# Kernel optimization log

Hardware: AMD Instinct MI355X
Metric: run time of the kernel (lower is better)

## Reference

```python
import jax, jax.numpy as jnp
import numpy as np

B, H, W, C = 8, 224, 224, 96
WS, SHIFT, HEADS = 7, 3, 3
N = WS * WS
HEAD_DIM = C // HEADS
SCALE = HEAD_DIM ** -0.5
EPS = 1e-5


def _build_shift_mask():
    # standard Swin shifted-window attention mask, values in {0, -100}
    img = np.zeros((H, W), np.float32)
    cnt = 0
    for hs in (slice(0, -WS), slice(-WS, -SHIFT), slice(-SHIFT, None)):
        for ws_ in (slice(0, -WS), slice(-WS, -SHIFT), slice(-SHIFT, None)):
            img[hs, ws_] = cnt
            cnt += 1
    mw = img.reshape(H // WS, WS, W // WS, WS).transpose(0, 2, 1, 3).reshape(-1, N)  # (nW, N)
    am = mw[:, None, :] - mw[:, :, None]
    am = np.where(am != 0, -100.0, 0.0).astype(np.float32)  # (nW, N, N)
    return np.tile(am, (B, 1, 1))  # (B*nW, N, N)


def setup_inputs() -> dict:
    key = jax.random.key(0)
    ks = jax.random.split(key, 6)
    s = 0.02
    return {
        "x": jax.random.normal(ks[0], (B, H, W, C), jnp.float32),
        "mask": jnp.asarray(_build_shift_mask()),
        "norm1_g": jnp.ones((C,), jnp.float32),
        "norm1_b": jnp.zeros((C,), jnp.float32),
        "qkv_w": jax.random.normal(ks[1], (3 * C, C), jnp.float32) * s,
        "qkv_b": jnp.zeros((3 * C,), jnp.float32),
        "proj_w": jax.random.normal(ks[2], (C, C), jnp.float32) * s,
        "proj_b": jnp.zeros((C,), jnp.float32),
        "norm2_g": jnp.ones((C,), jnp.float32),
        "norm2_b": jnp.zeros((C,), jnp.float32),
        "fc1_w": jax.random.normal(ks[3], (4 * C, C), jnp.float32) * s,
        "fc1_b": jnp.zeros((4 * C,), jnp.float32),
        "fc2_w": jax.random.normal(ks[4], (C, 4 * C), jnp.float32) * s,
        "fc2_b": jnp.zeros((C,), jnp.float32),
    }


def _ln(x, g, b):
    mu = jnp.mean(x, axis=-1, keepdims=True)
    var = jnp.mean(jnp.square(x - mu), axis=-1, keepdims=True)
    return (x - mu) * jax.lax.rsqrt(var + EPS) * g + b


def reference(x, mask, norm1_g, norm1_b, qkv_w, qkv_b, proj_w, proj_b,
              norm2_g, norm2_b, fc1_w, fc1_b, fc2_w, fc2_b):
    b, h, w, c = x.shape
    shortcut = x.reshape(b, h * w, c)
    xn = _ln(x, norm1_g, norm1_b)
    # cyclic shift
    xs = jnp.roll(xn, (-SHIFT, -SHIFT), axis=(1, 2))
    # window partition -> (B*nW, N, C)
    xw = xs.reshape(b, h // WS, WS, w // WS, WS, c).transpose(0, 1, 3, 2, 4, 5).reshape(-1, N, c)
    # window attention
    qkv = xw @ qkv_w.T + qkv_b                                  # (B_, N, 3C)
    qkv = qkv.reshape(-1, N, 3, HEADS, HEAD_DIM).transpose(2, 0, 3, 1, 4)
    q, k, v = qkv[0] * SCALE, qkv[1], qkv[2]                    # (B_, h, N, d)
    attn = jnp.einsum('bhnd,bhmd->bhnm', q, k) + mask[:, None]  # (B_, h, N, N)
    attn = jax.nn.softmax(attn, axis=-1)
    o = jnp.einsum('bhnm,bhmd->bhnd', attn, v).transpose(0, 2, 1, 3).reshape(-1, N, c)
    o = o @ proj_w.T + proj_b
    # window reverse
    o = o.reshape(b, h // WS, w // WS, WS, WS, c).transpose(0, 1, 3, 2, 4, 5).reshape(b, h, w, c)
    o = jnp.roll(o, (SHIFT, SHIFT), axis=(1, 2)).reshape(b, h * w, c)
    x = shortcut + o
    # MLP with exact (erf) GELU, as torch nn.GELU default
    y = _ln(x, norm2_g, norm2_b)
    y = jax.nn.gelu(y @ fc1_w.T + fc1_b, approximate=False)
    return x + (y @ fc2_w.T + fc2_b)
```

## Files before the change

kernel.cpp:

```cpp
#include <hip/hip_runtime.h>

typedef __attribute__((ext_vector_type(8))) short short8;
typedef __attribute__((ext_vector_type(4))) float floatx4;

#define MFMA(a,b,c) __builtin_amdgcn_mfma_f32_16x16x32_bf16(a,b,c,0,0,0)

__device__ __forceinline__ ushort f2bf(float f){ union{float f;uint i;}x; x.f=f; return (ushort)((x.i + 0x7fffu + ((x.i>>16)&1u))>>16); }
__device__ __forceinline__ short8 lds8(const ushort* p){ return *(const short8*)p; }

__global__ void convw_kernel(const float* __restrict__ qkvw,
                             const float* __restrict__ projw,
                             const float* __restrict__ f1w,
                             const float* __restrict__ f2w,
                             ushort* __restrict__ wb)
{
  int i = blockIdx.x*256 + threadIdx.x;
  float v;
  if      (i < 27648)  v = qkvw[i];
  else if (i < 36864)  v = projw[i-27648];
  else if (i < 73728)  v = f1w[i-36864];
  else if (i < 110592) v = f2w[i-73728];
  else return;
  wb[i] = f2bf(v);
}

__global__ __launch_bounds__(256,4) void swin_block_kernel(
    const float* __restrict__ x,
    const float* __restrict__ g1, const float* __restrict__ b1v,
    const ushort* __restrict__ qkv_wb, const float* __restrict__ qkv_b,
    const ushort* __restrict__ proj_wb, const float* __restrict__ proj_b,
    const float* __restrict__ g2, const float* __restrict__ b2v,
    const ushort* __restrict__ fc1_wb, const float* __restrict__ fc1_b,
    const ushort* __restrict__ fc2_wb, const float* __restrict__ fc2_b,
    float* __restrict__ out)
{
  __shared__ __align__(16) ushort sm[19200];
  __shared__ int sid[64];
  ushort* xn  = sm;
  ushort* Qh  = sm + 6656;
  ushort* Kh  = sm + 8704;
  ushort* Vh  = sm + 11264;
  ushort* Pb  = sm + 13568;
  float*  xrb = (float*)(sm + 6656);
  ushort* hb  = sm + 6656;

  const int tid  = threadIdx.x;
  const int w    = blockIdx.x;
  const int b    = w >> 10;
  const int wh   = (w >> 5) & 31;
  const int wwn  = w & 31;
  const int lane = tid & 63;
  const int wv   = tid >> 6;
  const int quad = lane >> 4;
  const int ln   = lane & 15;

  {
    const int n = tid >> 2, q = tid & 3;
    if (n < 49) {
      const int i = n / 7, j = n - 7*i;
      int hh = wh*7 + i + 3; if (hh >= 224) hh -= 224;
      int w2 = wwn*7 + j + 3; if (w2 >= 224) w2 -= 224;
      if (q == 0) {
        const int rr = (wh < 31) ? 0 : ((i < 4) ? 1 : 2);
        const int cr = (wwn < 31) ? 0 : ((j < 4) ? 1 : 2);
        sid[n] = rr*3 + cr;
      }
      const float* px = x + (((size_t)b*224 + hh)*224 + w2)*96 + q*24;
      float v[24]; float s = 0.f, s2 = 0.f;
      const float4* p4 = (const float4*)px;
      #pragma unroll
      for (int t = 0; t < 6; ++t) { float4 u = p4[t];
        v[t*4+0]=u.x; v[t*4+1]=u.y; v[t*4+2]=u.z; v[t*4+3]=u.w; }
      #pragma unroll
      for (int c = 0; c < 24; ++c) { s += v[c]; s2 += v[c]*v[c]; }
      s  += __shfl_xor(s, 1);  s  += __shfl_xor(s, 2);
      s2 += __shfl_xor(s2, 1); s2 += __shfl_xor(s2, 2);
      const float mu = s * (1.f/96.f);
      const float rs = rsqrtf(s2*(1.f/96.f) - mu*mu + 1e-5f);
      ushort* row = xn + n*104 + q*24;
      #pragma unroll
      for (int c = 0; c < 24; ++c)
        row[c] = f2bf((v[c]-mu)*rs*g1[q*24+c] + b1v[q*24+c]);
    }
    for (int idx = tid; idx < 15*104; idx += 256) xn[49*104 + idx] = 0;
  }
  __syncthreads();

  short8 a0, a1, a2;
  {
    const ushort* arow = xn + (wv*16 + ln)*104 + quad*8;
    a0 = lds8(arow); a1 = lds8(arow+32); a2 = lds8(arow+64);
  }
  int idrv[4], idcv[4];
  #pragma unroll
  for (int reg = 0; reg < 4; ++reg) {
    const int r = wv*16 + quad*4 + reg;
    idrv[reg] = (r < 49) ? sid[r] : -1;
  }
  #pragma unroll
  for (int nt = 0; nt < 4; ++nt) {
    const int c = nt*16 + ln;
    idcv[nt] = (c < 49) ? sid[c] : -2;
  }

  ushort* ob = xn;
  for (int h = 0; h < 3; ++h) {
    #pragma unroll
    for (int nt = 0; nt < 6; ++nt) {
      const int sec = nt >> 1, sub = nt & 1;
      const int colw = sec*96 + h*32 + sub*16 + ln;
      const ushort* wrow = qkv_wb + colw*96 + quad*8;
      floatx4 acc = {0.f,0.f,0.f,0.f};
      acc = MFMA(a0, lds8(wrow),    acc);
      acc = MFMA(a1, lds8(wrow+32), acc);
      acc = MFMA(a2, lds8(wrow+64), acc);
      const float bias = qkv_b[colw];
      const int d = sub*16 + ln;
      #pragma unroll
      for (int reg = 0; reg < 4; ++reg) {
        const int r = wv*16 + quad*4 + reg;
        float val = acc[reg] + bias;
        if (sec == 0)      Qh[r*32 + d] = f2bf(val * 0.17677669529663689f);
        else if (sec == 1) Kh[r*40 + d] = f2bf(val);
        else               Vh[d*72 + r] = f2bf(val);
      }
    }
    __syncthreads();

    {
      short8 aq = lds8(Qh + (wv*16 + ln)*32 + quad*8);
      floatx4 sc[4];
      #pragma unroll
      for (int nt = 0; nt < 4; ++nt) {
        short8 kb = lds8(Kh + (nt*16 + ln)*40 + quad*8);
        floatx4 z = {0.f,0.f,0.f,0.f};
        sc[nt] = MFMA(aq, kb, z);
      }
      #pragma unroll
      for (int reg = 0; reg < 4; ++reg) {
        float t[4]; float mx = -1e30f;
        #pragma unroll
        for (int nt = 0; nt < 4; ++nt) {
          float tv = -1e30f;
          if (idrv[reg] >= 0 && idcv[nt] >= 0)
            tv = sc[nt][reg] + ((idrv[reg] == idcv[nt]) ? 0.f : -100.f);
          t[nt] = tv; mx = fmaxf(mx, tv);
        }
        mx = fmaxf(mx, __shfl_xor(mx, 1));
        mx = fmaxf(mx, __shfl_xor(mx, 2));
        mx = fmaxf(mx, __shfl_xor(mx, 4));
        mx = fmaxf(mx, __shfl_xor(mx, 8));
        float e[4], sum = 0.f;
        #pragma unroll
        for (int nt = 0; nt < 4; ++nt) {
          e[nt] = (t[nt] > -1e29f) ? __expf(t[nt] - mx) : 0.f;
          sum += e[nt];
        }
        sum += __shfl_xor(sum, 1);
        sum += __shfl_xor(sum, 2);
        sum += __shfl_xor(sum, 4);
        sum += __shfl_xor(sum, 8);
        const float inv = (sum > 0.f) ? 1.f/sum : 0.f;
        #pragma unroll
        for (int nt = 0; nt < 4; ++nt)
          Pb[(wv*16 + quad*4 + reg)*72 + nt*16 + ln] = f2bf(e[nt]*inv);
      }
    }
    __syncthreads();

    {
      short8 p0 = lds8(Pb + (wv*16 + ln)*72 + quad*8);
      short8 p1 = lds8(Pb + (wv*16 + ln)*72 + 32 + quad*8);
      #pragma unroll
      for (int ntd = 0; ntd < 2; ++ntd) {
        floatx4 accO = {0.f,0.f,0.f,0.f};
        accO = MFMA(p0, lds8(Vh + (ntd*16+ln)*72 + quad*8),      accO);
        accO = MFMA(p1, lds8(Vh + (ntd*16+ln)*72 + 32 + quad*8), accO);
        #pragma unroll
        for (int reg = 0; reg < 4; ++reg)
          ob[(wv*16 + quad*4 + reg)*104 + h*32 + ntd*16 + ln] = f2bf(accO[reg]);
      }
    }
    __syncthreads();
  }

  {
    const ushort* arow = ob + (wv*16 + ln)*104 + quad*8;
    short8 o0 = lds8(arow), o1 = lds8(arow+32), o2 = lds8(arow+64);
    for (int nt = 0; nt < 6; ++nt) {
      const ushort* wrow = proj_wb + (nt*16 + ln)*96 + quad*8;
      floatx4 acc = {0.f,0.f,0.f,0.f};
      acc = MFMA(o0, lds8(wrow),    acc);
      acc = MFMA(o1, lds8(wrow+32), acc);
      acc = MFMA(o2, lds8(wrow+64), acc);
      const int col = nt*16 + ln;
      const float bias = proj_b[col];
      #pragma unroll
      for (int reg = 0; reg < 4; ++reg) {
        const int r = wv*16 + quad*4 + reg;
        if (r < 49) {
          const int i = r / 7, j = r - 7*i;
          int hh = wh*7 + i + 3; if (hh >= 224) hh -= 224;
          int w2 = wwn*7 + j + 3; if (w2 >= 224) w2 -= 224;
          const size_t pos = (((size_t)b*224 + hh)*224 + w2)*96 + col;
          const float val = x[pos] + acc[reg] + bias;
          xrb[r*96 + col] = val;
          out[pos] = val;
        }
      }
    }
    for (int idx = tid; idx < 15*96; idx += 256) xrb[49*96 + idx] = 0.f;
  }
  __syncthreads();

  {
    const int n = tid >> 2, q = tid & 3;
    const float4* p4 = (const float4*)(xrb + n*96 + q*24);
    float v[24]; float s = 0.f, s2 = 0.f;
    #pragma unroll
    for (int t = 0; t < 6; ++t) { float4 u = p4[t];
      v[t*4+0]=u.x; v[t*4+1]=u.y; v[t*4+2]=u.z; v[t*4+3]=u.w; }
    #pragma unroll
    for (int c = 0; c < 24; ++c) { s += v[c]; s2 += v[c]*v[c]; }
    s  += __shfl_xor(s, 1);  s  += __shfl_xor(s, 2);
    s2 += __shfl_xor(s2, 1); s2 += __shfl_xor(s2, 2);
    const float mu = s * (1.f/96.f);
    const float rs = rsqrtf(s2*(1.f/96.f) - mu*mu + 1e-5f);
    ushort* row = xn + n*104 + q*24;
    #pragma unroll
    for (int c = 0; c < 24; ++c)
      row[c] = f2bf((v[c]-mu)*rs*g2[q*24+c] + b2v[q*24+c]);
  }
  __syncthreads();

  const int rloc = (wv & 1) * 16;
  const int p    = wv >> 1;
  for (int half = 0; half < 2; ++half) {
    {
      const ushort* arow = xn + (half*32 + rloc + ln)*104 + quad*8;
      short8 m0 = lds8(arow), m1 = lds8(arow+32), m2 = lds8(arow+64);
      for (int t = 0; t < 12; ++t) {
        const int nt = p*12 + t;
        const ushort* wrow = fc1_wb + (nt*16 + ln)*96 + quad*8;
        floatx4 acc = {0.f,0.f,0.f,0.f};
        acc = MFMA(m0, lds8(wrow),    acc);
        acc = MFMA(m1, lds8(wrow+32), acc);
        acc = MFMA(m2, lds8(wrow+64), acc);
        const int col = nt*16 + ln;
        const float bias = fc1_b[col];
        #pragma unroll
        for (int reg = 0; reg < 4; ++reg) {
          const float vv = acc[reg] + bias;
          hb[(rloc + quad*4 + reg)*392 + col] =
              f2bf(0.5f*vv*(1.f + erff(vv*0.70710678118654752f)));
        }
      }
    }
    __syncthreads();
    {
      short8 ap[12];
      const ushort* prow = hb + (rloc + ln)*392 + quad*8;
      #pragma unroll
      for (int kt = 0; kt < 12; ++kt) ap[kt] = lds8(prow + kt*32);
      for (int t = 0; t < 3; ++t) {
        const int nt = p*3 + t;
        const ushort* wrow = fc2_wb + (nt*16 + ln)*384 + quad*8;
        floatx4 acc = {0.f,0.f,0.f,0.f};
        #pragma unroll
        for (int kt = 0; kt < 12; ++kt) acc = MFMA(ap[kt], lds8(wrow + kt*32), acc);
        const int col = nt*16 + ln;
        const float bias = fc2_b[col];
        #pragma unroll
        for (int reg = 0; reg < 4; ++reg) {
          const int r = half*32 + rloc + quad*4 + reg;
          if (r < 49) {
            const int i = r / 7, j = r - 7*i;
            int hh = wh*7 + i + 3; if (hh >= 224) hh -= 224;
            int w2 = wwn*7 + j + 3; if (w2 >= 224) w2 -= 224;
            const size_t pos = (((size_t)b*224 + hh)*224 + w2)*96 + col;
            out[pos] += acc[reg] + bias;
          }
        }
      }
    }
    __syncthreads();
  }
}

extern "C" void kernel_launch(void* const* d_in, const int* in_sizes, int n_in,
                              void* d_out, int out_size, void* d_ws, size_t ws_size,
                              hipStream_t stream) {
  int ix=-1, iq=-1, ip=-1, if1=-1, if2=-1, largest=0;
  for (int i = 0; i < n_in; ++i) {
    const int s = in_sizes[i];
    if (s == 38535168 && ix < 0) ix = i;
    else if (s == 27648 && iq < 0) iq = i;
    else if (s == 9216 && ip < 0) ip = i;
    else if (s == 36864) { if (if1 < 0) if1 = i; else if (if2 < 0) if2 = i; }
    if (in_sizes[i] >= in_sizes[largest]) largest = i;
  }
  if (ix < 0) ix = largest;
  if (iq < 0) iq = 4;
  if (ip < 0) ip = 6;
  if (if1 < 0) if1 = 10;
  if (if2 < 0) if2 = 12;

  const float* x    = (const float*)d_in[ix];
  const float* n1g  = (const float*)d_in[2];
  const float* n1b  = (const float*)d_in[3];
  const float* qkvw = (const float*)d_in[iq];
  const float* qkvb = (const float*)d_in[5];
  const float* pw   = (const float*)d_in[ip];
  const float* pb   = (const float*)d_in[7];
  const float* n2g  = (const float*)d_in[8];
  const float* n2b  = (const float*)d_in[9];
  const float* f1w  = (const float*)d_in[if1];
  const float* f1b  = (const float*)d_in[11];
  const float* f2w  = (const float*)d_in[if2];
  const float* f2b  = (const float*)d_in[13];
  float* outp = (float*)d_out;
  ushort* wb = (ushort*)d_ws;

  convw_kernel<<<432, 256, 0, stream>>>(qkvw, pw, f1w, f2w, wb);
  swin_block_kernel<<<8192, 256, 0, stream>>>(
      x, n1g, n1b, wb, qkvb, wb + 27648, pb,
      n2g, n2b, wb + 36864, f1b, wb + 73728, f2b, outp);
}
```

Baseline: 927.3 us.

## Re-tile GEMMs so each wave owns weight columns and reuses B fragments across row tiles

The QKV, proj, fc1 and fc2 GEMMs are restructured. Each wave now keeps all activation row-tiles in registers and loads each weight fragment once, reusing it across four row tiles, instead of reloading weights for every row tile. The MLP is split into two hidden chunks that accumulate fc2 results in registers, so out is read-modify-written only once and hb shrinks. Global output offsets are precomputed into shared memory. The cost is higher register pressure from 12-fragment arrays and accumulators, which may reduce occupancy under launch_bounds(256,4), plus some uneven work across waves for the V and proj tail tiles.

Measured after the change: 961.1 us. 1.04x slower.

```diff
diff --git a/kernel.cpp b/kernel.cpp
--- a/kernel.cpp
+++ b/kernel.cpp
@@ -34,13 +34,14 @@
     const ushort* __restrict__ fc2_wb, const float* __restrict__ fc2_b,
     float* __restrict__ out)
 {
-  __shared__ __align__(16) ushort sm[19200];
+  __shared__ __align__(16) ushort sm[19456];
   __shared__ int sid[64];
+  __shared__ int spos[64];
   ushort* xn  = sm;
   ushort* Qh  = sm + 6656;
-  ushort* Kh  = sm + 8704;
-  ushort* Vh  = sm + 11264;
-  ushort* Pb  = sm + 13568;
+  ushort* Kh  = sm + 9216;
+  ushort* Vh  = sm + 11776;
+  ushort* Pb  = sm + 14080;
   float*  xrb = (float*)(sm + 6656);
   ushort* hb  = sm + 6656;
 
@@ -63,9 +64,10 @@
       if (q == 0) {
         const int rr = (wh < 31) ? 0 : ((i < 4) ? 1 : 2);
         const int cr = (wwn < 31) ? 0 : ((j < 4) ? 1 : 2);
-        sid[n] = rr*3 + cr;
-      }
-      const float* px = x + (((size_t)b*224 + hh)*224 + w2)*96 + q*24;
+        sid[n]  = rr*3 + cr;
+        spos[n] = ((b*224 + hh)*224 + w2)*96;
+      }
+      const float* px = x + (size_t)(((b*224 + hh)*224 + w2)*96) + q*24;
       float v[24]; float s = 0.f, s2 = 0.f;
       const float4* p4 = (const float4*)px;
       #pragma unroll
@@ -86,11 +88,13 @@
   }
   __syncthreads();
 
-  short8 a0, a1, a2;
-  {
-    const ushort* arow = xn + (wv*16 + ln)*104 + quad*8;
-    a0 = lds8(arow); a1 = lds8(arow+32); a2 = lds8(arow+64);
-  }
+  short8 a_[12];
+  #pragma unroll
+  for (int rt = 0; rt < 4; ++rt)
+    #pragma unroll
+    for (int k = 0; k < 3; ++k)
+      a_[rt*3+k] = lds8(xn + (rt*16 + ln)*104 + k*32 + quad*8);
+
   int idrv[4], idcv[4];
   #pragma unroll
   for (int reg = 0; reg < 4; ++reg) {
@@ -105,30 +109,51 @@
 
   ushort* ob = xn;
   for (int h = 0; h < 3; ++h) {
-    #pragma unroll
-    for (int nt = 0; nt < 6; ++nt) {
-      const int sec = nt >> 1, sub = nt & 1;
+    {
+      const int sec  = wv >> 1;
+      const int sub  = wv & 1;
       const int colw = sec*96 + h*32 + sub*16 + ln;
-      const ushort* wrow = qkv_wb + colw*96 + quad*8;
-      floatx4 acc = {0.f,0.f,0.f,0.f};
-      acc = MFMA(a0, lds8(wrow),    acc);
-      acc = MFMA(a1, lds8(wrow+32), acc);
-      acc = MFMA(a2, lds8(wrow+64), acc);
-      const float bias = qkv_b[colw];
-      const int d = sub*16 + ln;
-      #pragma unroll
-      for (int reg = 0; reg < 4; ++reg) {
-        const int r = wv*16 + quad*4 + reg;
-        float val = acc[reg] + bias;
-        if (sec == 0)      Qh[r*32 + d] = f2bf(val * 0.17677669529663689f);
-        else if (sec == 1) Kh[r*40 + d] = f2bf(val);
-        else               Vh[d*72 + r] = f2bf(val);
+      const ushort* wr = qkv_wb + colw*96 + quad*8;
+      short8 b0 = lds8(wr), b1 = lds8(wr+32), b2 = lds8(wr+64);
+      const int colv = 192 + h*32 + (wv>>1)*16 + ln;
+      const ushort* wr2 = qkv_wb + colv*96 + quad*8;
+      short8 c0 = lds8(wr2), c1 = lds8(wr2+32), c2 = lds8(wr2+64);
+      const float biasA = qkv_b[colw];
+      const float biasV = qkv_b[colv];
+      const int d  = sub*16 + ln;
+      const int dv = (wv>>1)*16 + ln;
+      #pragma unroll
+      for (int rt = 0; rt < 4; ++rt) {
+        floatx4 acc = {0.f,0.f,0.f,0.f};
+        acc = MFMA(a_[rt*3+0], b0, acc);
+        acc = MFMA(a_[rt*3+1], b1, acc);
+        acc = MFMA(a_[rt*3+2], b2, acc);
+        #pragma unroll
+        for (int reg = 0; reg < 4; ++reg) {
+          const int r = rt*16 + quad*4 + reg;
+          const float val = acc[reg] + biasA;
+          if (sec == 0) Qh[r*40 + d] = f2bf(val * 0.17677669529663689f);
+          else          Kh[r*40 + d] = f2bf(val);
+        }
+      }
+      const int rt0 = (wv & 1)*2;
+      #pragma unroll
+      for (int j = 0; j < 2; ++j) {
+        floatx4 acc = {0.f,0.f,0.f,0.f};
+        acc = MFMA(a_[(rt0+j)*3+0], c0, acc);
+        acc = MFMA(a_[(rt0+j)*3+1], c1, acc);
+        acc = MFMA(a_[(rt0+j)*3+2], c2, acc);
+        #pragma unroll
+        for (int reg = 0; reg < 4; ++reg) {
+          const int r = (rt0+j)*16 + quad*4 + reg;
+          Vh[dv*72 + r] = f2bf(acc[reg] + biasV);
+        }
       }
     }
     __syncthreads();
 
     {
-      short8 aq = lds8(Qh + (wv*16 + ln)*32 + quad*8);
+      short8 aq = lds8(Qh + (wv*16 + ln)*40 + quad*8);
       floatx4 sc[4];
       #pragma unroll
       for (int nt = 0; nt < 4; ++nt) {
@@ -185,26 +210,52 @@
   }
 
   {
-    const ushort* arow = ob + (wv*16 + ln)*104 + quad*8;
-    short8 o0 = lds8(arow), o1 = lds8(arow+32), o2 = lds8(arow+64);
-    for (int nt = 0; nt < 6; ++nt) {
-      const ushort* wrow = proj_wb + (nt*16 + ln)*96 + quad*8;
+    short8 o_[12];
+    #pragma unroll
+    for (int rt = 0; rt < 4; ++rt)
+      #pragma unroll
+      for (int k = 0; k < 3; ++k)
+        o_[rt*3+k] = lds8(ob + (rt*16 + ln)*104 + k*32 + quad*8);
+
+    const int colA = wv*16 + ln;
+    const ushort* wr = proj_wb + colA*96 + quad*8;
+    short8 b0 = lds8(wr), b1 = lds8(wr+32), b2 = lds8(wr+64);
+    const int colB = (4 + (wv>>1))*16 + ln;
+    const ushort* wr2 = proj_wb + colB*96 + quad*8;
+    short8 c0 = lds8(wr2), c1 = lds8(wr2+32), c2 = lds8(wr2+64);
+    const float biasA = proj_b[colA], biasB = proj_b[colB];
+
+    #pragma unroll
+    for (int rt = 0; rt < 4; ++rt) {
       floatx4 acc = {0.f,0.f,0.f,0.f};
-      acc = MFMA(o0, lds8(wrow),    acc);
-      acc = MFMA(o1, lds8(wrow+32), acc);
-      acc = MFMA(o2, lds8(wrow+64), acc);
-      const int col = nt*16 + ln;
-      const float bias = proj_b[col];
+      acc = MFMA(o_[rt*3+0], b0, acc);
+      acc = MFMA(o_[rt*3+1], b1, acc);
+      acc = MFMA(o_[rt*3+2], b2, acc);
       #pragma unroll
       for (int reg = 0; reg < 4; ++reg) {
-        const int r = wv*16 + quad*4 + reg;
+        const int r = rt*16 + quad*4 + reg;
         if (r < 49) {
-          const int i = r / 7, j = r - 7*i;
-          int hh = wh*7 + i + 3; if (hh >= 224) hh -= 224;
-          int w2 = wwn*7 + j + 3; if (w2 >= 224) w2 -= 224;
-          const size_t pos = (((size_t)b*224 + hh)*224 + w2)*96 + col;
-          const float val = x[pos] + acc[reg] + bias;
-          xrb[r*96 + col] = val;
+          const int pos = spos[r] + colA;
+          const float val = x[pos] + acc[reg] + biasA;
+          xrb[r*96 + colA] = val;
+          out[pos] = val;
+        }
+      }
+    }
+    const int rt0 = (wv & 1)*2;
+    #pragma unroll
+    for (int j = 0; j < 2; ++j) {
+      floatx4 acc = {0.f,0.f,0.f,0.f};
+      acc = MFMA(o_[(rt0+j)*3+0], c0, acc);
+      acc = MFMA(o_[(rt0+j)*3+1], c1, acc);
+      acc = MFMA(o_[(rt0+j)*3+2], c2, acc);
+      #pragma unroll
+      for (int reg = 0; reg < 4; ++reg) {
+        const int r = (rt0+j)*16 + quad*4 + reg;
+        if (r < 49) {
+          const int pos = spos[r] + colB;
+          const float val = x[pos] + acc[reg] + biasB;
+          xrb[r*96 + colB] = val;
           out[pos] = val;
         }
       }
@@ -233,57 +284,91 @@
   }
   __syncthreads();
 
-  const int rloc = (wv & 1) * 16;
-  const int p    = wv >> 1;
-  for (int half = 0; half < 2; ++half) {
+  floatx4 Cacc[3][2];
+  #pragma unroll
+  for (int t = 0; t < 3; ++t)
+    #pragma unroll
+    for (int j = 0; j < 2; ++j)
+      Cacc[t][j] = (floatx4){0.f,0.f,0.f,0.f};
+  const int p  = wv >> 1;
+  const int cg = (wv & 1)*3;
+
+  for (int ch = 0; ch < 2; ++ch) {
     {
-      const ushort* arow = xn + (half*32 + rloc + ln)*104 + quad*8;
-      short8 m0 = lds8(arow), m1 = lds8(arow+32), m2 = lds8(arow+64);
-      for (int t = 0; t < 12; ++t) {
-        const int nt = p*12 + t;
-        const ushort* wrow = fc1_wb + (nt*16 + ln)*96 + quad*8;
-        floatx4 acc = {0.f,0.f,0.f,0.f};
-        acc = MFMA(m0, lds8(wrow),    acc);
-        acc = MFMA(m1, lds8(wrow+32), acc);
-        acc = MFMA(m2, lds8(wrow+64), acc);
-        const int col = nt*16 + ln;
-        const float bias = fc1_b[col];
-        #pragma unroll
-        for (int reg = 0; reg < 4; ++reg) {
-          const float vv = acc[reg] + bias;
-          hb[(rloc + quad*4 + reg)*392 + col] =
-              f2bf(0.5f*vv*(1.f + erff(vv*0.70710678118654752f)));
+      short8 m_[12];
+      #pragma unroll
+      for (int rt = 0; rt < 4; ++rt)
+        #pragma unroll
+        for (int k = 0; k < 3; ++k)
+          m_[rt*3+k] = lds8(xn + (rt*16 + ln)*104 + k*32 + quad*8);
+      #pragma unroll
+      for (int t = 0; t < 3; ++t) {
+        const int ntl  = wv*3 + t;
+        const int colh = ntl*16 + ln;
+        const int gcol = ch*192 + colh;
+        const ushort* wr1 = fc1_wb + gcol*96 + quad*8;
+        short8 b0 = lds8(wr1), b1 = lds8(wr1+32), b2 = lds8(wr1+64);
+        const float bias = fc1_b[gcol];
+        #pragma unroll
+        for (int rt = 0; rt < 4; ++rt) {
+          floatx4 acc = {0.f,0.f,0.f,0.f};
+          acc = MFMA(m_[rt*3+0], b0, acc);
+          acc = MFMA(m_[rt*3+1], b1, acc);
+          acc = MFMA(m_[rt*3+2], b2, acc);
+          #pragma unroll
+          for (int reg = 0; reg < 4; ++reg) {
+            const float vv = acc[reg] + bias;
+            hb[(rt*16 + quad*4 + reg)*200 + colh] =
+                f2bf(0.5f*vv*(1.f + erff(vv*0.70710678118654752f)));
+          }
         }
       }
     }
     __syncthreads();
     {
-      short8 ap[12];
-      const ushort* prow = hb + (rloc + ln)*392 + quad*8;
-      #pragma unroll
-      for (int kt = 0; kt < 12; ++kt) ap[kt] = lds8(prow + kt*32);
+      short8 h_[12];
+      #pragma unroll
+      for (int j = 0; j < 2; ++j)
+        #pragma unroll
+        for (int k = 0; k < 6; ++k)
+          h_[j*6+k] = lds8(hb + ((2*p+j)*16 + ln)*200 + k*32 + quad*8);
+      #pragma unroll
       for (int t = 0; t < 3; ++t) {
-        const int nt = p*3 + t;
-        const ushort* wrow = fc2_wb + (nt*16 + ln)*384 + quad*8;
-        floatx4 acc = {0.f,0.f,0.f,0.f};
-        #pragma unroll
-        for (int kt = 0; kt < 12; ++kt) acc = MFMA(ap[kt], lds8(wrow + kt*32), acc);
-        const int col = nt*16 + ln;
-        const float bias = fc2_b[col];
-        #pragma unroll
-        for (int reg = 0; reg < 4; ++reg) {
-          const int r = half*32 + rloc + quad*4 + reg;
-          if (r < 49) {
-            const int i = r / 7, j = r - 7*i;
-            int hh = wh*7 + i + 3; if (hh >= 224) hh -= 224;
-            int w2 = wwn*7 + j + 3; if (w2 >= 224) w2 -= 224;
-            const size_t pos = (((size_t)b*224 + hh)*224 + w2)*96 + col;
-            out[pos] += acc[reg] + bias;
-          }
+        const int outc = (cg + t)*16 + ln;
+        const ushort* wr2 = fc2_wb + outc*384 + ch*192 + quad*8;
+        short8 w0 = lds8(wr2),     w1 = lds8(wr2+32),  w2 = lds8(wr2+64),
+               w3 = lds8(wr2+96),  w4 = lds8(wr2+128), w5 = lds8(wr2+160);
+        #pragma unroll
+        for (int j = 0; j < 2; ++j) {
+          floatx4 acc = Cacc[t][j];
+          acc = MFMA(h_[j*6+0], w0, acc);
+          acc = MFMA(h_[j*6+1], w1, acc);
+          acc = MFMA(h_[j*6+2], w2, acc);
+          acc = MFMA(h_[j*6+3], w3, acc);
+          acc = MFMA(h_[j*6+4], w4, acc);
+          acc = MFMA(h_[j*6+5], w5, acc);
+          Cacc[t][j] = acc;
         }
       }
     }
     __syncthreads();
+  }
+
+  #pragma unroll
+  for (int t = 0; t < 3; ++t) {
+    const int outc = (cg + t)*16 + ln;
+    const float bias = fc2_b[outc];
+    #pragma unroll
+    for (int j = 0; j < 2; ++j) {
+      #pragma unroll
+      for (int reg = 0; reg < 4; ++reg) {
+        const int r = (2*p + j)*16 + quad*4 + reg;
+        if (r < 49) {
+          const int pos = spos[r] + outc;
+          out[pos] += Cacc[t][j][reg] + bias;
+        }
+      }
+    }
   }
 }
 
```
